# Kernel tuning notes

Measured on AMD Instinct MI355X. Metric: run time of the kernel, lower is better.

The kernel has to match this reference:

```python
import jax, jax.numpy as jnp
import numpy as np

N_CLASSES = 32000
K = 5          # LML budget N
TAU = 1.0
EPS_GATHER = 1e-8
N_BISECT = 60  # bisection iterations; bracket width ~42 -> resolved far below eps=1e-4


def lml_project(x, k):
    """Limited Multi-Label projection: p = sigmoid(x + nu) with nu s.t. sum_j p_j = k.
    nu* found per-row by bisection (monotone in nu), followed by one differentiable
    Newton step so gradients match the implicit-function-theorem backward of LML.
    x: [B, C] -> p: [B, C].
    """
    xs = jax.lax.stop_gradient(x)
    # sum sigmoid(x+nu) is increasing in nu; these brackets guarantee a sign change
    lo = -jnp.max(xs, axis=-1, keepdims=True) - 20.0  # [B,1], g(lo) < 0
    hi = -jnp.min(xs, axis=-1, keepdims=True) + 20.0  # [B,1], g(hi) > 0

    def body(i, lh):
        lo, hi = lh
        mid = 0.5 * (lo + hi)
        g = jnp.sum(jax.nn.sigmoid(xs + mid), axis=-1, keepdims=True) - k
        lo = jnp.where(g < 0, mid, lo)
        hi = jnp.where(g < 0, hi, mid)
        return (lo, hi)

    lo, hi = jax.lax.fori_loop(0, N_BISECT, body, (lo, hi))
    nu = 0.5 * (lo + hi)

    # one differentiable Newton step at the converged root (identity in value,
    # yields exact implicit gradient dnu/dx = -sig'/sum(sig'))
    s = jax.nn.sigmoid(x + nu)
    g = jnp.sum(s, axis=-1, keepdims=True) - k
    gp = jnp.sum(s * (1.0 - s), axis=-1, keepdims=True)
    nu = nu - g / gp
    return jax.nn.sigmoid(x + nu)


def setup_inputs() -> dict:
    key = jax.random.key(0)
    k1, k2 = jax.random.split(key)
    x = jax.random.normal(k1, (2048, N_CLASSES), dtype=jnp.float32)
    y = jax.random.randint(k2, (2048,), 0, N_CLASSES)
    return {"x": x, "y": y}


def reference(x, y):
    # F.normalize(x): L2 normalize rows with eps=1e-12
    norm = jnp.sqrt(jnp.sum(x * x, axis=-1, keepdims=True))
    xn = x / jnp.maximum(norm, 1e-12)
    p = lml_project(xn / TAU, K)                      # [B, C]
    py = jnp.take_along_axis(p, y[:, None], axis=1)   # [B, 1]
    return jnp.mean(-jnp.log(py + EPS_GATHER))
```

## Files before the change

kernel.cpp:

```cpp
#include <hip/hip_runtime.h>
#include <math.h>

#define CDIM 32000
#define KVAL 5.0f
#define EPS_GATHER 1e-8f

#define NT 640
#define NW (NT / 64)
#define PER 50
#define NEWTON_ITERS 2

__device__ __forceinline__ float frcp(float x) { return __builtin_amdgcn_rcpf(x); }

__device__ __forceinline__ void block_allreduce2(float a, float b,
                                                 float* s_pa, float* s_pb,
                                                 float* s_r, int t,
                                                 float& oa, float& ob) {
#pragma unroll
    for (int o = 32; o > 0; o >>= 1) {
        a += __shfl_down(a, o, 64);
        b += __shfl_down(b, o, 64);
    }
    const int wid = t >> 6;
    if ((t & 63) == 0) { s_pa[wid] = a; s_pb[wid] = b; }
    __syncthreads();
    if (t == 0) {
        float ra = 0.f, rb = 0.f;
#pragma unroll
        for (int w = 0; w < NW; ++w) { ra += s_pa[w]; rb += s_pb[w]; }
        s_r[0] = ra; s_r[1] = rb;
    }
    __syncthreads();
    oa = s_r[0];
    ob = s_r[1];
}

__global__ __launch_bounds__(NT) void lml_rows(const float* __restrict__ x,
                                               const int* __restrict__ y,
                                               float* __restrict__ row_loss,
                                               int nrows) {
    __shared__ float s_pa[NW], s_pb[NW], s_r[2];
    const int row = blockIdx.x;
    if (row >= nrows) return;
    const int t = threadIdx.x;
    const float* xr = x + (long long)row * CDIM;

    float v[PER];
    float ss = 0.f;
#pragma unroll
    for (int i = 0; i < PER / 2; ++i) {
        float2 d = *(const float2*)(xr + (2 * t + i * (2 * NT)));
        v[2 * i] = d.x;
        v[2 * i + 1] = d.y;
        ss = fmaf(d.x, d.x, ss);
        ss = fmaf(d.y, d.y, ss);
    }
    float tot_ss, dummy;
    block_allreduce2(ss, 0.f, s_pa, s_pb, s_r, t, tot_ss, dummy);

    const float norm = sqrtf(tot_ss);
    const float rnorm = 1.0f / fmaxf(norm, 1e-12f);
#pragma unroll
    for (int i = 0; i < PER; ++i) v[i] *= rnorm;

    float se = 0.f;
#pragma unroll
    for (int i = 0; i < PER; ++i) se += __expf(v[i]);
    float S;
    block_allreduce2(se, 0.f, s_pa, s_pb, s_r, t, S, dummy);
    float nu = logf(KVAL) - logf(S);

    for (int it = 0; it < NEWTON_ITERS; ++it) {
        float g = 0.f, gp = 0.f;
#pragma unroll
        for (int i = 0; i < PER; ++i) {
            const float e = __expf(v[i] + nu);
            const float s = e * frcp(1.f + e);
            g += s;
            gp = fmaf(s, 1.f - s, gp);
        }
        float G, GP;
        block_allreduce2(g, gp, s_pa, s_pb, s_r, t, G, GP);
        nu -= (G - KVAL) / GP;
    }

    if (t == 0) {
        const int yi = y[row];
        const float xn_y = xr[yi] * rnorm;
        const float e = __expf(xn_y + nu);
        const float p = e / (1.f + e);
        row_loss[row] = -logf(p + EPS_GATHER);
    }
}

__global__ __launch_bounds__(1024) void mean_kernel(const float* __restrict__ row_loss,
                                                    float* __restrict__ out, int nrows) {
    __shared__ float s_p[16];
    const int t = threadIdx.x;
    float s = 0.f;
    for (int i = t; i < nrows; i += 1024) s += row_loss[i];
#pragma unroll
    for (int o = 32; o > 0; o >>= 1) s += __shfl_down(s, o, 64);
    if ((t & 63) == 0) s_p[t >> 6] = s;
    __syncthreads();
    if (t == 0) {
        float tot = 0.f;
#pragma unroll
        for (int w = 0; w < 16; ++w) tot += s_p[w];
        out[0] = tot / (float)nrows;
    }
}

extern "C" void kernel_launch(void* const* d_in, const int* in_sizes, int n_in,
                              void* d_out, int out_size, void* d_ws, size_t ws_size,
                              hipStream_t stream) {
    const float* x = (const float*)d_in[0];
    const int* y = (const int*)d_in[1];
    float* out = (float*)d_out;
    const int nrows = in_sizes[1];
    float* row_loss = (float*)d_ws;

    lml_rows<<<nrows, NT, 0, stream>>>(x, y, row_loss, nrows);
    mean_kernel<<<1, 1024, 0, stream>>>(row_loss, out, nrows);
}
```

Before: 403.9 us.

## Replace per-element Newton sweeps with moment-based series solve for nu

Computes three power sums of exp(xn) in a single pass and solves for a=exp(nu) with a scalar Newton iteration on a third-order series expansion of the sigmoid sum. This removes the repeated exp/sigmoid sweeps and block reductions of the Newton iterations. The row is reread from memory instead of held in registers, and the block size is halved with float4 loads. The accuracy relies on a*exp(xn) being small, which holds for normalized rows with many classes.

```diff
diff --git a/kernel.cpp b/kernel.cpp
--- a/kernel.cpp
+++ b/kernel.cpp
@@ -5,90 +5,95 @@
 #define KVAL 5.0f
 #define EPS_GATHER 1e-8f
 
-#define NT 640
+#define NT 320
 #define NW (NT / 64)
-#define PER 50
-#define NEWTON_ITERS 2
+#define PER4 25
 
-__device__ __forceinline__ float frcp(float x) { return __builtin_amdgcn_rcpf(x); }
-
-__device__ __forceinline__ void block_allreduce2(float a, float b,
-                                                 float* s_pa, float* s_pb,
-                                                 float* s_r, int t,
-                                                 float& oa, float& ob) {
-#pragma unroll
-    for (int o = 32; o > 0; o >>= 1) {
-        a += __shfl_down(a, o, 64);
-        b += __shfl_down(b, o, 64);
-    }
-    const int wid = t >> 6;
-    if ((t & 63) == 0) { s_pa[wid] = a; s_pb[wid] = b; }
-    __syncthreads();
-    if (t == 0) {
-        float ra = 0.f, rb = 0.f;
-#pragma unroll
-        for (int w = 0; w < NW; ++w) { ra += s_pa[w]; rb += s_pb[w]; }
-        s_r[0] = ra; s_r[1] = rb;
-    }
-    __syncthreads();
-    oa = s_r[0];
-    ob = s_r[1];
-}
 
 __global__ __launch_bounds__(NT) void lml_rows(const float* __restrict__ x,
                                                const int* __restrict__ y,
                                                float* __restrict__ row_loss,
                                                int nrows) {
-    __shared__ float s_pa[NW], s_pb[NW], s_r[2];
+    __shared__ float s_p[3 * NW];
+    __shared__ float s_r[1];
     const int row = blockIdx.x;
     if (row >= nrows) return;
     const int t = threadIdx.x;
-    const float* xr = x + (long long)row * CDIM;
+    const float4* __restrict__ xr4 = (const float4*)(x + (long long)row * CDIM);
 
-    float v[PER];
     float ss = 0.f;
-#pragma unroll
-    for (int i = 0; i < PER / 2; ++i) {
-        float2 d = *(const float2*)(xr + (2 * t + i * (2 * NT)));
-        v[2 * i] = d.x;
-        v[2 * i + 1] = d.y;
+#pragma unroll 5
+    for (int i = 0; i < PER4; ++i) {
+        const float4 d = xr4[t + i * NT];
         ss = fmaf(d.x, d.x, ss);
         ss = fmaf(d.y, d.y, ss);
+        ss = fmaf(d.z, d.z, ss);
+        ss = fmaf(d.w, d.w, ss);
     }
-    float tot_ss, dummy;
-    block_allreduce2(ss, 0.f, s_pa, s_pb, s_r, t, tot_ss, dummy);
+#pragma unroll
+    for (int o = 32; o > 0; o >>= 1) ss += __shfl_down(ss, o, 64);
+    if ((t & 63) == 0) s_p[t >> 6] = ss;
+    __syncthreads();
+    if (t == 0) {
+        float r = 0.f;
+#pragma unroll
+        for (int w = 0; w < NW; ++w) r += s_p[w];
+        s_r[0] = r;
+    }
+    __syncthreads();
+    const float rnorm = 1.0f / fmaxf(sqrtf(s_r[0]), 1e-12f);
+    __syncthreads();
 
-    const float norm = sqrtf(tot_ss);
-    const float rnorm = 1.0f / fmaxf(norm, 1e-12f);
+    float m1 = 0.f, m2 = 0.f, m3 = 0.f;
+#pragma unroll 5
+    for (int i = 0; i < PER4; ++i) {
+        const float4 d = xr4[t + i * NT];
+        {
+            const float e = __expf(d.x * rnorm);
+            m1 += e; m2 = fmaf(e, e, m2); m3 = fmaf(e * e, e, m3);
+        }
+        {
+            const float e = __expf(d.y * rnorm);
+            m1 += e; m2 = fmaf(e, e, m2); m3 = fmaf(e * e, e, m3);
+        }
+        {
+            const float e = __expf(d.z * rnorm);
+            m1 += e; m2 = fmaf(e, e, m2); m3 = fmaf(e * e, e, m3);
+        }
+        {
+            const float e = __expf(d.w * rnorm);
+            m1 += e; m2 = fmaf(e, e, m2); m3 = fmaf(e * e, e, m3);
+        }
+    }
 #pragma unroll
-    for (int i = 0; i < PER; ++i) v[i] *= rnorm;
-
-    float se = 0.f;
-#pragma unroll
-    for (int i = 0; i < PER; ++i) se += __expf(v[i]);
-    float S;
-    block_allreduce2(se, 0.f, s_pa, s_pb, s_r, t, S, dummy);
-    float nu = logf(KVAL) - logf(S);
-
-    for (int it = 0; it < NEWTON_ITERS; ++it) {
-        float g = 0.f, gp = 0.f;
-#pragma unroll
-        for (int i = 0; i < PER; ++i) {
-            const float e = __expf(v[i] + nu);
-            const float s = e * frcp(1.f + e);
-            g += s;
-            gp = fmaf(s, 1.f - s, gp);
-        }
-        float G, GP;
-        block_allreduce2(g, gp, s_pa, s_pb, s_r, t, G, GP);
-        nu -= (G - KVAL) / GP;
+    for (int o = 32; o > 0; o >>= 1) {
+        m1 += __shfl_down(m1, o, 64);
+        m2 += __shfl_down(m2, o, 64);
+        m3 += __shfl_down(m3, o, 64);
     }
+    if ((t & 63) == 0) {
+        const int w = t >> 6;
+        s_p[w] = m1; s_p[NW + w] = m2; s_p[2 * NW + w] = m3;
+    }
+    __syncthreads();
 
     if (t == 0) {
+        float S1 = 0.f, S2 = 0.f, S3 = 0.f;
+#pragma unroll
+        for (int w = 0; w < NW; ++w) {
+            S1 += s_p[w]; S2 += s_p[NW + w]; S3 += s_p[2 * NW + w];
+        }
+        float a = KVAL / S1;
+#pragma unroll
+        for (int it = 0; it < 4; ++it) {
+            const float g = a * (S1 - a * (S2 - a * S3)) - KVAL;
+            const float gp = S1 - a * (2.f * S2 - 3.f * a * S3);
+            a -= g / gp;
+        }
         const int yi = y[row];
-        const float xn_y = xr[yi] * rnorm;
-        const float e = __expf(xn_y + nu);
-        const float p = e / (1.f + e);
+        const float ev = __expf(x[(long long)row * CDIM + yi] * rnorm);
+        const float ae = a * ev;
+        const float p = ae / (1.f + ae);
         row_loss[row] = -logf(p + EPS_GATHER);
     }
 }
```

After: 373.4 us. -7.6%, faster.
